# Optimization experiments

Measured on AMD Instinct MI355X. Metric: run time of the kernel, lower is better.

## Reference

```python
import jax, jax.numpy as jnp
import numpy as np

N = 100_000      # nodes in batched candidate graph
P = 150_000      # undirected bonds
E = 2 * P        # directed edges; edge 2i=(u,v), 2i+1=(v,u)
M = 10_000       # tree messages scattered onto edges
DN, DE, DM, DX = 256, 64, 256, 256
ITERS = 3


def setup_inputs() -> dict:
    key = jax.random.key(0)
    ks = jax.random.split(key, 12)
    f_node = jax.random.normal(ks[0], (N, DN), jnp.float32)
    f_edge = jax.random.normal(ks[1], (E, DE), jnp.float32)
    src_p = jax.random.randint(ks[2], (P,), 0, N, dtype=jnp.int32)
    dst_p = jax.random.randint(ks[3], (P,), 0, N, dtype=jnp.int32)
    edge_src = jnp.stack([src_p, dst_p], axis=1).reshape(-1)  # [E]
    edge_dst = jnp.stack([dst_p, src_p], axis=1).reshape(-1)  # [E]
    tree_msg = jax.random.normal(ks[4], (M, DM), jnp.float32)
    tree_tgt = (jnp.arange(M, dtype=jnp.int32) * (E // M))    # unique target edge ids
    s = lambda d: np.float32(1.0 / np.sqrt(d))
    W1 = jax.random.normal(ks[5], (DN, DM), jnp.float32) * s(DN)
    W2 = jax.random.normal(ks[6], (DE, DM), jnp.float32) * s(DE)
    W3 = jax.random.normal(ks[7], (DM, DM), jnp.float32) * s(DM)
    b1 = jnp.zeros((DM,), jnp.float32)
    W4 = jax.random.normal(ks[8], (DN, DX), jnp.float32) * s(DN)
    W5 = jax.random.normal(ks[9], (DM, DX), jnp.float32) * s(DM)
    b2 = jnp.zeros((DX,), jnp.float32)
    return dict(f_node=f_node, f_edge=f_edge, tree_msg=tree_msg,
                W1=W1, W2=W2, W3=W3, b1=b1, W4=W4, W5=W5, b2=b2,
                edge_src=edge_src, edge_dst=edge_dst, tree_tgt=tree_tgt)


def reference(f_node, f_edge, tree_msg, W1, W2, W3, b1, W4, W5, b2,
              edge_src, edge_dst, tree_tgt):
    n_nodes = f_node.shape[0]
    n_edges = f_edge.shape[0]
    d_msg = W3.shape[0]
    # scatter tree messages into per-edge alpha (edata['alpha'])
    alpha = jnp.zeros((n_edges, d_msg), f_node.dtype).at[tree_tgt].set(tree_msg)
    # g1_G static part: W1 f_src + W2 f_edge + b1 (constant across iterations)
    base = f_node[edge_src] @ W1 + f_edge @ W2 + b1  # [E, DM]
    rev = jnp.arange(n_edges) ^ 1  # reverse edge of e (pairs stored consecutively)
    msg = jnp.zeros((n_edges, d_msg), f_node.dtype)
    for _ in range(ITERS):
        # line-graph (backtracking=False) copy_src + sum reduce:
        # sum over incoming edges (w,u) of e=(u,v) excluding w==v
        agg = jax.ops.segment_sum(msg, edge_dst, num_segments=n_nodes)  # [N, DM]
        sum_msg = agg[edge_src] - msg[rev]
        msg = jax.nn.relu(base + (sum_msg + alpha) @ W3)
    # readout: copy_edge + sum per destination node, then g2_G
    node_sum = jax.ops.segment_sum(msg, edge_dst, num_segments=n_nodes)  # [N, DM]
    x = jax.nn.relu(f_node @ W4 + node_sum @ W5 + b2)  # [N, DX]
    return x
```

## Files before the change

### kernel.cpp

```cpp
#include <hip/hip_runtime.h>
#include <hip/hip_bf16.h>

typedef __hip_bfloat16 bf16;
typedef __bf16 bf16x8 __attribute__((ext_vector_type(8)));
typedef __bf16 bf16x4 __attribute__((ext_vector_type(4)));
typedef float f32x4 __attribute__((ext_vector_type(4)));

#define DN_ 256
#define DE_ 64
#define DM_ 256
#define DX_ 256
#define LDH 136
#define LDA2 72
#define CAP 32


static __device__ __forceinline__ bf16 f2b(float x) { return __float2bfloat16(x); }
static __device__ __forceinline__ float us2f(unsigned short u) {
    return __uint_as_float((unsigned)u << 16);
}

union U16x8 { uint4 u; unsigned short s[8]; };

static __device__ __forceinline__ f32x4 mfma16(bf16x8 a, bf16x8 b, f32x4 c) {
    return __builtin_amdgcn_mfma_f32_16x16x32_bf16(a, b, c, 0, 0, 0);
}

template <int LDA, int WSTR, int KLEN>
static __device__ __forceinline__ void gemm_acc(const bf16* T, const bf16* WT,
                                                f32x4 acc[4][4], int lane, int wave) {
    const int m = lane & 15, quad = lane >> 4;
#pragma unroll
    for (int k0 = 0; k0 < KLEN; k0 += 32) {
        bf16x8 a[4], b[4];
#pragma unroll
        for (int i = 0; i < 4; ++i)
            a[i] = *(const bf16x8*)&T[(i * 16 + m) * LDA + k0 + quad * 8];
#pragma unroll
        for (int j = 0; j < 4; ++j) {
            int n = wave * 64 + j * 16 + m;
            b[j] = *(const bf16x8*)&WT[(size_t)n * WSTR + k0 + quad * 8];
        }
#pragma unroll
        for (int i = 0; i < 4; ++i)
#pragma unroll
            for (int j = 0; j < 4; ++j)
                acc[i][j] = mfma16(b[j], a[i], acc[i][j]);
    }
}

__global__ void __launch_bounds__(256) k_transpose(const float* __restrict__ W,
                                                   bf16* __restrict__ WT, int K, int NC) {
    int i = blockIdx.x * 256 + threadIdx.x;
    if (i < K * NC) {
        int k = i / NC, n = i % NC;
        WT[n * K + k] = f2b(W[i]);
    }
}

__global__ void __launch_bounds__(256) k_cvt(const float* __restrict__ in,
                                             bf16* __restrict__ out, long total) {
    long i = ((long)blockIdx.x * 256 + threadIdx.x) * 8;
    if (i >= total) return;
    float4 v0 = *(const float4*)(in + i);
    float4 v1 = *(const float4*)(in + i + 4);
    bf16x8 b = {(__bf16)v0.x, (__bf16)v0.y, (__bf16)v0.z, (__bf16)v0.w,
                (__bf16)v1.x, (__bf16)v1.y, (__bf16)v1.z, (__bf16)v1.w};
    *(bf16x8*)(out + i) = b;
}

__global__ void __launch_bounds__(256) k_bucket(const int* __restrict__ edst,
                                                int* __restrict__ cnt,
                                                int* __restrict__ slot, int E) {
    int e = blockIdx.x * 256 + threadIdx.x;
    if (e < E) {
        int d = edst[e];
        int pos = atomicAdd(&cnt[d], 1);
        if (pos < CAP) slot[(size_t)d * CAP + pos] = e;
    }
}

__global__ void __launch_bounds__(256) k_invset(const int* __restrict__ tgt,
                                                int* __restrict__ inv, int M) {
    int r = blockIdx.x * 256 + threadIdx.x;
    if (r < M) inv[tgt[r]] = r;
}

__global__ void __launch_bounds__(256) k_aggregate(const bf16* __restrict__ msg,
                                                   const int* __restrict__ cnt,
                                                   const int* __restrict__ slot,
                                                   bf16* __restrict__ agg, int N,
                                                   int relu_in) {
    int wid = (blockIdx.x * 256 + threadIdx.x) >> 6;
    int lane = threadIdx.x & 63;
    if (wid >= N) return;
    int c = cnt[wid];
    if (c > CAP) c = CAP;
    const int* sp = slot + (size_t)wid * CAP;
    float a0 = 0.f, a1 = 0.f, a2 = 0.f, a3 = 0.f;
    if (relu_in) {
        for (int i = 0; i < c; ++i) {
            int e = sp[i];
            ushort4 mv = *(const ushort4*)((const unsigned short*)msg + (size_t)e * DM_ + lane * 4);
            a0 += fmaxf(us2f(mv.x), 0.f); a1 += fmaxf(us2f(mv.y), 0.f);
            a2 += fmaxf(us2f(mv.z), 0.f); a3 += fmaxf(us2f(mv.w), 0.f);
        }
    } else {
        for (int i = 0; i < c; ++i) {
            int e = sp[i];
            ushort4 mv = *(const ushort4*)((const unsigned short*)msg + (size_t)e * DM_ + lane * 4);
            a0 += us2f(mv.x); a1 += us2f(mv.y); a2 += us2f(mv.z); a3 += us2f(mv.w);
        }
    }
    bf16x4 o = {(__bf16)a0, (__bf16)a1, (__bf16)a2, (__bf16)a3};
    *(bf16x4*)(agg + (size_t)wid * DM_ + lane * 4) = o;
}

__global__ void __launch_bounds__(256) k_alpha(const float* __restrict__ tm,
                                               const bf16* __restrict__ W3T,
                                               bf16* __restrict__ alpha3, int M) {
    __shared__ bf16 T[64 * LDH];
    const int tile0 = blockIdx.x * 64, tid = threadIdx.x;
    const int lane = tid & 63, wave = tid >> 6;
    const int m = lane & 15, quad = lane >> 4;
    f32x4 acc[4][4];
#pragma unroll
    for (int i = 0; i < 4; ++i)
#pragma unroll
        for (int j = 0; j < 4; ++j) acc[i][j] = (f32x4){0.f, 0.f, 0.f, 0.f};
#pragma unroll
    for (int h = 0; h < 2; ++h) {
#pragma unroll
        for (int it = 0; it < 8; ++it) {
            int c = tid + it * 256;
            int r = c >> 5, cc = c & 31;
            int row = tile0 + r;
            if (row >= M) row = 0;
            float4 v = *(const float4*)(tm + (size_t)row * DM_ + h * 128 + cc * 4);
            bf16x4 b = {(__bf16)v.x, (__bf16)v.y, (__bf16)v.z, (__bf16)v.w};
            *(bf16x4*)&T[r * LDH + cc * 4] = b;
        }
        __syncthreads();
        gemm_acc<LDH, 256, 128>(T, W3T + h * 128, acc, lane, wave);
        __syncthreads();
    }
#pragma unroll
    for (int i = 0; i < 4; ++i) {
        int row = tile0 + i * 16 + m;
        if (row < M) {
            size_t rb = (size_t)row * DM_;
#pragma unroll
            for (int j = 0; j < 4; ++j) {
                int c0 = wave * 64 + j * 16 + quad * 4;
                bf16x4 o = {(__bf16)acc[i][j][0], (__bf16)acc[i][j][1],
                            (__bf16)acc[i][j][2], (__bf16)acc[i][j][3]};
                *(bf16x4*)(alpha3 + rb + c0) = o;
            }
        }
    }
}

__global__ void __launch_bounds__(256) k_base(const bf16* __restrict__ fnb,
                                              const float* __restrict__ fedge,
                                              const int* __restrict__ esrc,
                                              const bf16* __restrict__ W1T,
                                              const bf16* __restrict__ W2T,
                                              const float* __restrict__ b1,
                                              const int* __restrict__ inv,
                                              const bf16* __restrict__ alpha3,
                                              bf16* __restrict__ base2, int E) {
    __shared__ bf16 T[64 * LDH];
    const int tile0 = blockIdx.x * 64, tid = threadIdx.x;
    const int lane = tid & 63, wave = tid >> 6;
    const int m = lane & 15, quad = lane >> 4;
    f32x4 acc[4][4];
#pragma unroll
    for (int i = 0; i < 4; ++i)
#pragma unroll
        for (int j = 0; j < 4; ++j) acc[i][j] = (f32x4){0.f, 0.f, 0.f, 0.f};
#pragma unroll
    for (int h = 0; h < 2; ++h) {
#pragma unroll
        for (int it = 0; it < 4; ++it) {
            int c = tid + it * 256;
            int r = c >> 4, cc = c & 15;
            int e = tile0 + r;
            if (e >= E) e = 0;
            int s = esrc[e];
            *(uint4*)&T[r * LDH + cc * 8] =
                *(const uint4*)((const unsigned short*)fnb + (size_t)s * DN_ + h * 128 + cc * 8);
        }
        __syncthreads();
        gemm_acc<LDH, 256, 128>(T, W1T + h * 128, acc, lane, wave);
        __syncthreads();
    }
#pragma unroll
    for (int it = 0; it < 4; ++it) {
        int c = tid + it * 256;
        int r = c >> 4, cc = c & 15;
        int e = tile0 + r;
        if (e >= E) e = 0;
        float4 v = *(const float4*)(fedge + (size_t)e * DE_ + cc * 4);
        bf16x4 b = {(__bf16)v.x, (__bf16)v.y, (__bf16)v.z, (__bf16)v.w};
        *(bf16x4*)&T[r * LDA2 + cc * 4] = b;
    }
    __syncthreads();
    gemm_acc<LDA2, 64, 64>(T, W2T, acc, lane, wave);
    float4 bj[4];
#pragma unroll
    for (int j = 0; j < 4; ++j)
        bj[j] = *(const float4*)&b1[wave * 64 + j * 16 + quad * 4];
#pragma unroll
    for (int i = 0; i < 4; ++i) {
        int e = tile0 + i * 16 + m;
        if (e < E) {
            int iv = inv[e];
            size_t rb = (size_t)e * DM_;
#pragma unroll
            for (int j = 0; j < 4; ++j) {
                int c0 = wave * 64 + j * 16 + quad * 4;
                float v0 = acc[i][j][0] + bj[j].x;
                float v1 = acc[i][j][1] + bj[j].y;
                float v2 = acc[i][j][2] + bj[j].z;
                float v3 = acc[i][j][3] + bj[j].w;
                if (iv >= 0) {
                    ushort4 al = *(const ushort4*)((const unsigned short*)alpha3 +
                                                   (size_t)iv * DM_ + c0);
                    v0 += us2f(al.x); v1 += us2f(al.y);
                    v2 += us2f(al.z); v3 += us2f(al.w);
                }
                bf16x4 o = {(__bf16)v0, (__bf16)v1, (__bf16)v2, (__bf16)v3};
                *(bf16x4*)(base2 + rb + c0) = o;
            }
        }
    }
}

__global__ void __launch_bounds__(256) k_update(const bf16* __restrict__ agg,
                                                const bf16* __restrict__ base2,
                                                const int* __restrict__ esrc,
                                                const bf16* __restrict__ W3T,
                                                const bf16* __restrict__ msgin,
                                                bf16* __restrict__ msgout, int E,
                                                int relu_in) {
    __shared__ bf16 T[64 * LDH];
    const int tile0 = blockIdx.x * 64, tid = threadIdx.x;
    const int lane = tid & 63, wave = tid >> 6;
    const int m = lane & 15, quad = lane >> 4;
    f32x4 acc[4][4];
#pragma unroll
    for (int i = 0; i < 4; ++i)
#pragma unroll
        for (int j = 0; j < 4; ++j) acc[i][j] = (f32x4){0.f, 0.f, 0.f, 0.f};
#pragma unroll
    for (int h = 0; h < 2; ++h) {
#pragma unroll
        for (int it = 0; it < 4; ++it) {
            int c = tid + it * 256;
            int r = c >> 4, cc = c & 15;
            int e = tile0 + r;
            int ec = e < E ? e : 0;
            int s = esrc[ec];
            int erev = tile0 + (r ^ 1);
            if (erev >= E) erev = 0;
            U16x8 av, mv;
            av.u = *(const uint4*)((const unsigned short*)agg +
                                   (size_t)s * DM_ + h * 128 + cc * 8);
            mv.u = *(const uint4*)((const unsigned short*)msgin +
                                   (size_t)erev * DM_ + h * 128 + cc * 8);
            bf16x8 o;
#pragma unroll
            for (int t = 0; t < 8; ++t) {
                float fm = us2f(mv.s[t]);
                if (relu_in) fm = fmaxf(fm, 0.f);
                o[t] = (__bf16)(us2f(av.s[t]) - fm);
            }
            *(bf16x8*)&T[r * LDH + cc * 8] = o;
        }
        __syncthreads();
        gemm_acc<LDH, 256, 128>(T, W3T + h * 128, acc, lane, wave);
        __syncthreads();
    }
#pragma unroll
    for (int i = 0; i < 4; ++i) {
        int e = tile0 + i * 16 + m;
        if (e < E) {
            size_t rb = (size_t)e * DM_;
#pragma unroll
            for (int j = 0; j < 4; ++j) {
                int c0 = wave * 64 + j * 16 + quad * 4;
                ushort4 bv = *(const ushort4*)((const unsigned short*)base2 + rb + c0);
                float v0 = fmaxf(acc[i][j][0] + us2f(bv.x), 0.f);
                float v1 = fmaxf(acc[i][j][1] + us2f(bv.y), 0.f);
                float v2 = fmaxf(acc[i][j][2] + us2f(bv.z), 0.f);
                float v3 = fmaxf(acc[i][j][3] + us2f(bv.w), 0.f);
                bf16x4 o = {(__bf16)v0, (__bf16)v1, (__bf16)v2, (__bf16)v3};
                *(bf16x4*)(msgout + rb + c0) = o;
            }
        }
    }
}

__global__ void __launch_bounds__(256) k_readout(const float* __restrict__ fnode,
                                                 const bf16* __restrict__ agg,
                                                 const bf16* __restrict__ W4T,
                                                 const bf16* __restrict__ W5T,
                                                 const float* __restrict__ b2,
                                                 float* __restrict__ out, int N) {
    __shared__ bf16 T[64 * LDH];
    const int tile0 = blockIdx.x * 64, tid = threadIdx.x;
    const int lane = tid & 63, wave = tid >> 6;
    const int m = lane & 15, quad = lane >> 4;
    f32x4 acc[4][4];
#pragma unroll
    for (int i = 0; i < 4; ++i)
#pragma unroll
        for (int j = 0; j < 4; ++j) acc[i][j] = (f32x4){0.f, 0.f, 0.f, 0.f};
#pragma unroll
    for (int h = 0; h < 2; ++h) {
#pragma unroll
        for (int it = 0; it < 8; ++it) {
            int c = tid + it * 256;
            int r = c >> 5, cc = c & 31;
            int n = tile0 + r;
            if (n >= N) n = 0;
            float4 v = *(const float4*)(fnode + (size_t)n * DN_ + h * 128 + cc * 4);
            bf16x4 b = {(__bf16)v.x, (__bf16)v.y, (__bf16)v.z, (__bf16)v.w};
            *(bf16x4*)&T[r * LDH + cc * 4] = b;
        }
        __syncthreads();
        gemm_acc<LDH, 256, 128>(T, W4T + h * 128, acc, lane, wave);
        __syncthreads();
    }
#pragma unroll
    for (int h = 0; h < 2; ++h) {
#pragma unroll
        for (int it = 0; it < 4; ++it) {
            int c = tid + it * 256;
            int r = c >> 4, cc = c & 15;
            int n = tile0 + r;
            if (n >= N) n = 0;
            *(uint4*)&T[r * LDH + cc * 8] =
                *(const uint4*)((const unsigned short*)agg + (size_t)n * DM_ + h * 128 + cc * 8);
        }
        __syncthreads();
        gemm_acc<LDH, 256, 128>(T, W5T + h * 128, acc, lane, wave);
        __syncthreads();
    }
    float4 bj[4];
#pragma unroll
    for (int j = 0; j < 4; ++j)
        bj[j] = *(const float4*)&b2[wave * 64 + j * 16 + quad * 4];
#pragma unroll
    for (int i = 0; i < 4; ++i) {
        int n = tile0 + i * 16 + m;
        if (n < N) {
            size_t rb = (size_t)n * DX_;
#pragma unroll
            for (int j = 0; j < 4; ++j) {
                int c0 = wave * 64 + j * 16 + quad * 4;
                float4 o;
                o.x = fmaxf(acc[i][j][0] + bj[j].x, 0.f);
                o.y = fmaxf(acc[i][j][1] + bj[j].y, 0.f);
                o.z = fmaxf(acc[i][j][2] + bj[j].z, 0.f);
                o.w = fmaxf(acc[i][j][3] + bj[j].w, 0.f);
                *(float4*)(out + rb + c0) = o;
            }
        }
    }
}

extern "C" void kernel_launch(void* const* d_in, const int* in_sizes, int n_in,
                              void* d_out, int out_size, void* d_ws, size_t ws_size,
                              hipStream_t stream) {
    const float* f_node   = (const float*)d_in[0];
    const float* f_edge   = (const float*)d_in[1];
    const float* tree_msg = (const float*)d_in[2];
    const float* W1 = (const float*)d_in[3];
    const float* W2 = (const float*)d_in[4];
    const float* W3 = (const float*)d_in[5];
    const float* b1 = (const float*)d_in[6];
    const float* W4 = (const float*)d_in[7];
    const float* W5 = (const float*)d_in[8];
    const float* b2 = (const float*)d_in[9];
    const int* edge_src = (const int*)d_in[10];
    const int* edge_dst = (const int*)d_in[11];
    const int* tree_tgt = (const int*)d_in[12];

    const int N = in_sizes[0] / DN_;
    const int E = in_sizes[1] / DE_;
    const int M = in_sizes[2] / DM_;

    char* ws = (char*)d_ws;
    size_t off = 0;
    bf16* base2 = (bf16*)(ws + off); off += (size_t)E * DM_ * 2;
    bf16* msg   = (bf16*)(ws + off); off += (size_t)E * DM_ * 2;
    bf16* agg   = (bf16*)(ws + off); off += (size_t)N * DM_ * 2;
    int* cnt    = (int*)(ws + off);   off += (size_t)N * 4;
    int* slot   = (int*)(ws + off);   off += (size_t)N * CAP * 4;
    int* inv    = (int*)(ws + off);   off += (size_t)E * 4;
    bf16* alpha3 = (bf16*)(ws + off); off += (size_t)M * DM_ * 2;
    bf16* W1T = (bf16*)(ws + off); off += 256 * 256 * 2;
    bf16* W2T = (bf16*)(ws + off); off += 256 * 64 * 2;
    bf16* W3T = (bf16*)(ws + off); off += 256 * 256 * 2;
    bf16* W4T = (bf16*)(ws + off); off += 256 * 256 * 2;
    bf16* W5T = (bf16*)(ws + off); off += 256 * 256 * 2;
    bf16* fnb = msg;

    k_transpose<<<(256 * 256 + 255) / 256, 256, 0, stream>>>(W1, W1T, 256, 256);
    k_transpose<<<(64 * 256 + 255) / 256, 256, 0, stream>>>(W2, W2T, 64, 256);
    k_transpose<<<(256 * 256 + 255) / 256, 256, 0, stream>>>(W3, W3T, 256, 256);
    k_transpose<<<(256 * 256 + 255) / 256, 256, 0, stream>>>(W4, W4T, 256, 256);
    k_transpose<<<(256 * 256 + 255) / 256, 256, 0, stream>>>(W5, W5T, 256, 256);

    hipMemsetAsync(cnt, 0, (size_t)N * 4, stream);
    hipMemsetAsync(inv, 0xFF, (size_t)E * 4, stream);
    k_bucket<<<(E + 255) / 256, 256, 0, stream>>>(edge_dst, cnt, slot, E);
    k_invset<<<(M + 255) / 256, 256, 0, stream>>>(tree_tgt, inv, M);

    k_cvt<<<(int)(((size_t)N * DN_ / 8 + 255) / 256), 256, 0, stream>>>(
        f_node, fnb, (long)N * DN_);

    k_alpha<<<(M + 63) / 64, 256, 0, stream>>>(tree_msg, W3T, alpha3, M);
    k_base<<<(E + 63) / 64, 256, 0, stream>>>(fnb, f_edge, edge_src, W1T, W2T, b1,
                                              inv, alpha3, base2, E);
    k_aggregate<<<(N + 3) / 4, 256, 0, stream>>>(base2, cnt, slot, agg, N, 1);
    k_update<<<(E + 63) / 64, 256, 0, stream>>>(agg, base2, edge_src, W3T,
                                                base2, msg, E, 1);
    k_aggregate<<<(N + 3) / 4, 256, 0, stream>>>(msg, cnt, slot, agg, N, 0);
    k_update<<<(E + 63) / 64, 256, 0, stream>>>(agg, base2, edge_src, W3T,
                                                msg, msg, E, 0);
    k_aggregate<<<(N + 3) / 4, 256, 0, stream>>>(msg, cnt, slot, agg, N, 0);
    k_readout<<<(N + 63) / 64, 256, 0, stream>>>(f_node, agg, W4T, W5T, b2,
                                                 (float*)d_out, N);
}
```

Measured before the change: 1.085 ms.

## Propagate W3-projected messages via linearity and fuse final update into readout

Because aggregation and reverse-edge subtraction are linear, the code now aggregates messages already multiplied by W3 (m3) instead of raw messages. k_base computes relu(base)·W3 directly, each update becomes relu(base + agg3[src] − m3[rev]) fed into the next W3 GEMM, and the last message update is fused into the readout gather, which removes one full edge GEMM pass and the final E×256 message write. The cost is heavier gathers in readout (base2, m3 and agg3 per incoming edge) and a larger shared-memory tile in k_base. Precision changes because products are rounded to bf16 before they are summed.

```diff
diff --git a/kernel.cpp b/kernel.cpp
--- a/kernel.cpp
+++ b/kernel.cpp
@@ -10,6 +10,7 @@
 #define DE_ 64
 #define DM_ 256
 #define DX_ 256
+#define LDF 264
 #define LDH 136
 #define LDA2 72
 #define CAP 32
@@ -86,11 +87,10 @@
     if (r < M) inv[tgt[r]] = r;
 }
 
-__global__ void __launch_bounds__(256) k_aggregate(const bf16* __restrict__ msg,
+__global__ void __launch_bounds__(256) k_aggregate(const bf16* __restrict__ m3,
                                                    const int* __restrict__ cnt,
                                                    const int* __restrict__ slot,
-                                                   bf16* __restrict__ agg, int N,
-                                                   int relu_in) {
+                                                   bf16* __restrict__ agg3, int N) {
     int wid = (blockIdx.x * 256 + threadIdx.x) >> 6;
     int lane = threadIdx.x & 63;
     if (wid >= N) return;
@@ -98,22 +98,19 @@
     if (c > CAP) c = CAP;
     const int* sp = slot + (size_t)wid * CAP;
     float a0 = 0.f, a1 = 0.f, a2 = 0.f, a3 = 0.f;
-    if (relu_in) {
-        for (int i = 0; i < c; ++i) {
-            int e = sp[i];
-            ushort4 mv = *(const ushort4*)((const unsigned short*)msg + (size_t)e * DM_ + lane * 4);
-            a0 += fmaxf(us2f(mv.x), 0.f); a1 += fmaxf(us2f(mv.y), 0.f);
-            a2 += fmaxf(us2f(mv.z), 0.f); a3 += fmaxf(us2f(mv.w), 0.f);
-        }
-    } else {
-        for (int i = 0; i < c; ++i) {
-            int e = sp[i];
-            ushort4 mv = *(const ushort4*)((const unsigned short*)msg + (size_t)e * DM_ + lane * 4);
+    if (c > 0) {
+        ushort4 mv = *(const ushort4*)((const unsigned short*)m3 +
+                                       (size_t)sp[0] * DM_ + lane * 4);
+        for (int i = 1; i < c; ++i) {
+            ushort4 nv = *(const ushort4*)((const unsigned short*)m3 +
+                                           (size_t)sp[i] * DM_ + lane * 4);
             a0 += us2f(mv.x); a1 += us2f(mv.y); a2 += us2f(mv.z); a3 += us2f(mv.w);
-        }
+            mv = nv;
+        }
+        a0 += us2f(mv.x); a1 += us2f(mv.y); a2 += us2f(mv.z); a3 += us2f(mv.w);
     }
     bf16x4 o = {(__bf16)a0, (__bf16)a1, (__bf16)a2, (__bf16)a3};
-    *(bf16x4*)(agg + (size_t)wid * DM_ + lane * 4) = o;
+    *(bf16x4*)(agg3 + (size_t)wid * DM_ + lane * 4) = o;
 }
 
 __global__ void __launch_bounds__(256) k_alpha(const float* __restrict__ tm,
@@ -168,8 +165,10 @@
                                               const float* __restrict__ b1,
                                               const int* __restrict__ inv,
                                               const bf16* __restrict__ alpha3,
-                                              bf16* __restrict__ base2, int E) {
-    __shared__ bf16 T[64 * LDH];
+                                              const bf16* __restrict__ W3T,
+                                              bf16* __restrict__ base2,
+                                              bf16* __restrict__ m3, int E) {
+    __shared__ bf16 T[64 * LDF];
     const int tile0 = blockIdx.x * 64, tid = threadIdx.x;
     const int lane = tid & 63, wave = tid >> 6;
     const int m = lane & 15, quad = lane >> 4;
@@ -206,43 +205,65 @@
     }
     __syncthreads();
     gemm_acc<LDA2, 64, 64>(T, W2T, acc, lane, wave);
+    __syncthreads();
     float4 bj[4];
 #pragma unroll
     for (int j = 0; j < 4; ++j)
         bj[j] = *(const float4*)&b1[wave * 64 + j * 16 + quad * 4];
+#pragma unroll
+    for (int i = 0; i < 4; ++i) {
+        int e = tile0 + i * 16 + m;
+        int iv = (e < E) ? inv[e] : -1;
+        size_t rb = (size_t)e * DM_;
+#pragma unroll
+        for (int j = 0; j < 4; ++j) {
+            int c0 = wave * 64 + j * 16 + quad * 4;
+            float v0 = acc[i][j][0] + bj[j].x;
+            float v1 = acc[i][j][1] + bj[j].y;
+            float v2 = acc[i][j][2] + bj[j].z;
+            float v3 = acc[i][j][3] + bj[j].w;
+            if (iv >= 0) {
+                ushort4 al = *(const ushort4*)((const unsigned short*)alpha3 +
+                                               (size_t)iv * DM_ + c0);
+                v0 += us2f(al.x); v1 += us2f(al.y);
+                v2 += us2f(al.z); v3 += us2f(al.w);
+            }
+            if (e < E) {
+                bf16x4 o = {(__bf16)v0, (__bf16)v1, (__bf16)v2, (__bf16)v3};
+                *(bf16x4*)(base2 + rb + c0) = o;
+            }
+            bf16x4 rl = {(__bf16)fmaxf(v0, 0.f), (__bf16)fmaxf(v1, 0.f),
+                         (__bf16)fmaxf(v2, 0.f), (__bf16)fmaxf(v3, 0.f)};
+            *(bf16x4*)&T[(i * 16 + m) * LDF + c0] = rl;
+        }
+    }
+    __syncthreads();
+#pragma unroll
+    for (int i = 0; i < 4; ++i)
+#pragma unroll
+        for (int j = 0; j < 4; ++j) acc[i][j] = (f32x4){0.f, 0.f, 0.f, 0.f};
+    gemm_acc<LDF, 256, 256>(T, W3T, acc, lane, wave);
 #pragma unroll
     for (int i = 0; i < 4; ++i) {
         int e = tile0 + i * 16 + m;
         if (e < E) {
-            int iv = inv[e];
             size_t rb = (size_t)e * DM_;
 #pragma unroll
             for (int j = 0; j < 4; ++j) {
                 int c0 = wave * 64 + j * 16 + quad * 4;
-                float v0 = acc[i][j][0] + bj[j].x;
-                float v1 = acc[i][j][1] + bj[j].y;
-                float v2 = acc[i][j][2] + bj[j].z;
-                float v3 = acc[i][j][3] + bj[j].w;
-                if (iv >= 0) {
-                    ushort4 al = *(const ushort4*)((const unsigned short*)alpha3 +
-                                                   (size_t)iv * DM_ + c0);
-                    v0 += us2f(al.x); v1 += us2f(al.y);
-                    v2 += us2f(al.z); v3 += us2f(al.w);
-                }
-                bf16x4 o = {(__bf16)v0, (__bf16)v1, (__bf16)v2, (__bf16)v3};
-                *(bf16x4*)(base2 + rb + c0) = o;
-            }
-        }
-    }
-}
-
-__global__ void __launch_bounds__(256) k_update(const bf16* __restrict__ agg,
-                                                const bf16* __restrict__ base2,
+                bf16x4 o = {(__bf16)acc[i][j][0], (__bf16)acc[i][j][1],
+                            (__bf16)acc[i][j][2], (__bf16)acc[i][j][3]};
+                *(bf16x4*)(m3 + rb + c0) = o;
+            }
+        }
+    }
+}
+
+__global__ void __launch_bounds__(256) k_gemm3f(const bf16* __restrict__ base2,
+                                                const bf16* __restrict__ agg3,
                                                 const int* __restrict__ esrc,
                                                 const bf16* __restrict__ W3T,
-                                                const bf16* __restrict__ msgin,
-                                                bf16* __restrict__ msgout, int E,
-                                                int relu_in) {
+                                                bf16* __restrict__ m3, int E) {
     __shared__ bf16 T[64 * LDH];
     const int tile0 = blockIdx.x * 64, tid = threadIdx.x;
     const int lane = tid & 63, wave = tid >> 6;
@@ -254,27 +275,33 @@
         for (int j = 0; j < 4; ++j) acc[i][j] = (f32x4){0.f, 0.f, 0.f, 0.f};
 #pragma unroll
     for (int h = 0; h < 2; ++h) {
+        uint4 bv[4], av[4], mv[4];
 #pragma unroll
         for (int it = 0; it < 4; ++it) {
             int c = tid + it * 256;
             int r = c >> 4, cc = c & 15;
             int e = tile0 + r;
-            int ec = e < E ? e : 0;
-            int s = esrc[ec];
+            if (e >= E) e = 0;
+            int s = esrc[e];
             int erev = tile0 + (r ^ 1);
             if (erev >= E) erev = 0;
-            U16x8 av, mv;
-            av.u = *(const uint4*)((const unsigned short*)agg +
-                                   (size_t)s * DM_ + h * 128 + cc * 8);
-            mv.u = *(const uint4*)((const unsigned short*)msgin +
-                                   (size_t)erev * DM_ + h * 128 + cc * 8);
+            bv[it] = *(const uint4*)((const unsigned short*)base2 +
+                                     (size_t)e * DM_ + h * 128 + cc * 8);
+            av[it] = *(const uint4*)((const unsigned short*)agg3 +
+                                     (size_t)s * DM_ + h * 128 + cc * 8);
+            mv[it] = *(const uint4*)((const unsigned short*)m3 +
+                                     (size_t)erev * DM_ + h * 128 + cc * 8);
+        }
+#pragma unroll
+        for (int it = 0; it < 4; ++it) {
+            int c = tid + it * 256;
+            int r = c >> 4, cc = c & 15;
+            U16x8 b, a, mm;
+            b.u = bv[it]; a.u = av[it]; mm.u = mv[it];
             bf16x8 o;
 #pragma unroll
-            for (int t = 0; t < 8; ++t) {
-                float fm = us2f(mv.s[t]);
-                if (relu_in) fm = fmaxf(fm, 0.f);
-                o[t] = (__bf16)(us2f(av.s[t]) - fm);
-            }
+            for (int t = 0; t < 8; ++t)
+                o[t] = (__bf16)fmaxf(us2f(b.s[t]) + us2f(a.s[t]) - us2f(mm.s[t]), 0.f);
             *(bf16x8*)&T[r * LDH + cc * 8] = o;
         }
         __syncthreads();
@@ -289,25 +316,26 @@
 #pragma unroll
             for (int j = 0; j < 4; ++j) {
                 int c0 = wave * 64 + j * 16 + quad * 4;
-                ushort4 bv = *(const ushort4*)((const unsigned short*)base2 + rb + c0);
-                float v0 = fmaxf(acc[i][j][0] + us2f(bv.x), 0.f);
-                float v1 = fmaxf(acc[i][j][1] + us2f(bv.y), 0.f);
-                float v2 = fmaxf(acc[i][j][2] + us2f(bv.z), 0.f);
-                float v3 = fmaxf(acc[i][j][3] + us2f(bv.w), 0.f);
-                bf16x4 o = {(__bf16)v0, (__bf16)v1, (__bf16)v2, (__bf16)v3};
-                *(bf16x4*)(msgout + rb + c0) = o;
+                bf16x4 o = {(__bf16)acc[i][j][0], (__bf16)acc[i][j][1],
+                            (__bf16)acc[i][j][2], (__bf16)acc[i][j][3]};
+                *(bf16x4*)(m3 + rb + c0) = o;
             }
         }
     }
 }
 
 __global__ void __launch_bounds__(256) k_readout(const float* __restrict__ fnode,
-                                                 const bf16* __restrict__ agg,
+                                                 const bf16* __restrict__ base2,
+                                                 const bf16* __restrict__ m3,
+                                                 const bf16* __restrict__ agg3,
+                                                 const int* __restrict__ esrc,
+                                                 const int* __restrict__ cnt,
+                                                 const int* __restrict__ slot,
                                                  const bf16* __restrict__ W4T,
                                                  const bf16* __restrict__ W5T,
                                                  const float* __restrict__ b2,
                                                  float* __restrict__ out, int N) {
-    __shared__ bf16 T[64 * LDH];
+    __shared__ bf16 T[64 * LDF];
     const int tile0 = blockIdx.x * 64, tid = threadIdx.x;
     const int lane = tid & 63, wave = tid >> 6;
     const int m = lane & 15, quad = lane >> 4;
@@ -332,21 +360,34 @@
         gemm_acc<LDH, 256, 128>(T, W4T + h * 128, acc, lane, wave);
         __syncthreads();
     }
-#pragma unroll
-    for (int h = 0; h < 2; ++h) {
-#pragma unroll
-        for (int it = 0; it < 4; ++it) {
-            int c = tid + it * 256;
-            int r = c >> 4, cc = c & 15;
-            int n = tile0 + r;
-            if (n >= N) n = 0;
-            *(uint4*)&T[r * LDH + cc * 8] =
-                *(const uint4*)((const unsigned short*)agg + (size_t)n * DM_ + h * 128 + cc * 8);
-        }
-        __syncthreads();
-        gemm_acc<LDH, 256, 128>(T, W5T + h * 128, acc, lane, wave);
-        __syncthreads();
-    }
+    for (int i = 0; i < 16; ++i) {
+        int r = wave * 16 + i;
+        int n = tile0 + r;
+        float a0 = 0.f, a1 = 0.f, a2 = 0.f, a3 = 0.f;
+        if (n < N) {
+            int c = cnt[n];
+            if (c > CAP) c = CAP;
+            const int* sp = slot + (size_t)n * CAP;
+            for (int t = 0; t < c; ++t) {
+                int er = sp[t];
+                int s = esrc[er];
+                ushort4 bv = *(const ushort4*)((const unsigned short*)base2 +
+                                               (size_t)er * DM_ + lane * 4);
+                ushort4 mv = *(const ushort4*)((const unsigned short*)m3 +
+                                               (size_t)(er ^ 1) * DM_ + lane * 4);
+                ushort4 av = *(const ushort4*)((const unsigned short*)agg3 +
+                                               (size_t)s * DM_ + lane * 4);
+                a0 += fmaxf(us2f(bv.x) + us2f(av.x) - us2f(mv.x), 0.f);
+                a1 += fmaxf(us2f(bv.y) + us2f(av.y) - us2f(mv.y), 0.f);
+                a2 += fmaxf(us2f(bv.z) + us2f(av.z) - us2f(mv.z), 0.f);
+                a3 += fmaxf(us2f(bv.w) + us2f(av.w) - us2f(mv.w), 0.f);
+            }
+        }
+        bf16x4 o = {(__bf16)a0, (__bf16)a1, (__bf16)a2, (__bf16)a3};
+        *(bf16x4*)&T[r * LDF + lane * 4] = o;
+    }
+    __syncthreads();
+    gemm_acc<LDF, 256, 256>(T, W5T, acc, lane, wave);
     float4 bj[4];
 #pragma unroll
     for (int j = 0; j < 4; ++j)
@@ -394,8 +435,8 @@
     char* ws = (char*)d_ws;
     size_t off = 0;
     bf16* base2 = (bf16*)(ws + off); off += (size_t)E * DM_ * 2;
-    bf16* msg   = (bf16*)(ws + off); off += (size_t)E * DM_ * 2;
-    bf16* agg   = (bf16*)(ws + off); off += (size_t)N * DM_ * 2;
+    bf16* m3    = (bf16*)(ws + off); off += (size_t)E * DM_ * 2;
+    bf16* agg3  = (bf16*)(ws + off); off += (size_t)N * DM_ * 2;
     int* cnt    = (int*)(ws + off);   off += (size_t)N * 4;
     int* slot   = (int*)(ws + off);   off += (size_t)N * CAP * 4;
     int* inv    = (int*)(ws + off);   off += (size_t)E * 4;
@@ -405,7 +446,7 @@
     bf16* W3T = (bf16*)(ws + off); off += 256 * 256 * 2;
     bf16* W4T = (bf16*)(ws + off); off += 256 * 256 * 2;
     bf16* W5T = (bf16*)(ws + off); off += 256 * 256 * 2;
-    bf16* fnb = msg;
+    bf16* fnb = agg3;
 
     k_transpose<<<(256 * 256 + 255) / 256, 256, 0, stream>>>(W1, W1T, 256, 256);
     k_transpose<<<(64 * 256 + 255) / 256, 256, 0, stream>>>(W2, W2T, 64, 256);
@@ -423,14 +464,11 @@
 
     k_alpha<<<(M + 63) / 64, 256, 0, stream>>>(tree_msg, W3T, alpha3, M);
     k_base<<<(E + 63) / 64, 256, 0, stream>>>(fnb, f_edge, edge_src, W1T, W2T, b1,
-                                              inv, alpha3, base2, E);
-    k_aggregate<<<(N + 3) / 4, 256, 0, stream>>>(base2, cnt, slot, agg, N, 1);
-    k_update<<<(E + 63) / 64, 256, 0, stream>>>(agg, base2, edge_src, W3T,
-                                                base2, msg, E, 1);
-    k_aggregate<<<(N + 3) / 4, 256, 0, stream>>>(msg, cnt, slot, agg, N, 0);
-    k_update<<<(E + 63) / 64, 256, 0, stream>>>(agg, base2, edge_src, W3T,
-                                                msg, msg, E, 0);
-    k_aggregate<<<(N + 3) / 4, 256, 0, stream>>>(msg, cnt, slot, agg, N, 0);
-    k_readout<<<(N + 63) / 64, 256, 0, stream>>>(f_node, agg, W4T, W5T, b2,
+                                              inv, alpha3, W3T, base2, m3, E);
+    k_aggregate<<<(N + 3) / 4, 256, 0, stream>>>(m3, cnt, slot, agg3, N);
+    k_gemm3f<<<(E + 63) / 64, 256, 0, stream>>>(base2, agg3, edge_src, W3T, m3, E);
+    k_aggregate<<<(N + 3) / 4, 256, 0, stream>>>(m3, cnt, slot, agg3, N);
+    k_readout<<<(N + 63) / 64, 256, 0, stream>>>(f_node, base2, m3, agg3, edge_src,
+                                                 cnt, slot, W4T, W5T, b2,
                                                  (float*)d_out, N);
 }
```

Measured after the change: 1.193 ms. 9.9% more time.
